# Kernel tuning notes

Measured on AMD Instinct MI355X. Metric: run time of the kernel, lower is better.

## Reference

```python
import jax, jax.numpy as jnp
import numpy as np

B, N, C = 8, 4096, 512
H = 8
OUT = 512
DH = C // H  # 64
LN_EPS = 1e-5
L2_EPS = 1e-12


def setup_inputs() -> dict:
    key = jax.random.key(0)
    ks = jax.random.split(key, 6)
    x = jax.random.normal(ks[0], (B, N, C), dtype=jnp.float32)
    ln_g = jnp.ones((C,), dtype=jnp.float32)
    ln_b = jnp.zeros((C,), dtype=jnp.float32)
    qkv_w = jax.random.normal(ks[1], (3 * C, C), dtype=jnp.float32) * 0.02  # torch Linear weight [out,in]
    temperature = jnp.ones((H, 1, 1), dtype=jnp.float32)
    proj_w = jax.random.normal(ks[2], (OUT, C), dtype=jnp.float32) * 0.02
    proj_b = jnp.zeros((OUT,), dtype=jnp.float32)
    return {"x": x, "ln_g": ln_g, "ln_b": ln_b, "qkv_w": qkv_w,
            "temperature": temperature, "proj_w": proj_w, "proj_b": proj_b}


def reference(x, ln_g, ln_b, qkv_w, temperature, proj_w, proj_b):
    # LayerNorm
    mu = jnp.mean(x, axis=-1, keepdims=True)
    var = jnp.mean(jnp.square(x - mu), axis=-1, keepdims=True)
    xn = (x - mu) * jax.lax.rsqrt(var + LN_EPS) * ln_g + ln_b
    # QKV projection (no bias)
    qkv = xn @ qkv_w.T  # [B,N,3C]
    qkv = qkv.reshape(B, N, 3, H, DH).transpose(2, 0, 3, 4, 1)  # [3,B,H,DH,N]
    q, k, v = qkv[0], qkv[1], qkv[2]  # each [B,H,DH,N] (already 'transposed' channel layout)
    # L2-normalize q,k along token dim (matches F.normalize eps behavior)
    q = q / jnp.clip(jnp.linalg.norm(q, axis=-1, keepdims=True), L2_EPS)
    k = k / jnp.clip(jnp.linalg.norm(k, axis=-1, keepdims=True), L2_EPS)
    # channel attention [B,H,DH,DH], scaled by per-head temperature
    attn = jnp.einsum('bhdn,bhen->bhde', q, k) * temperature[None]
    attn = jax.nn.softmax(attn, axis=-1)
    out = jnp.einsum('bhde,bhen->bhdn', attn, v)  # [B,H,DH,N]
    out = out.transpose(0, 3, 1, 2).reshape(B, N, H * DH)  # [B,N,C]
    out = jax.nn.gelu(out, approximate=False)
    out = out @ proj_w.T + proj_b
    return out
```

## Files before the change

### kernel.cpp

```cpp
#include <hip/hip_runtime.h>
#include <hip/hip_bf16.h>

typedef __hip_bfloat16 bf16;
typedef __bf16 bfrag __attribute__((ext_vector_type(8)));
typedef float f32x4 __attribute__((ext_vector_type(4)));

#define AS1 __attribute__((address_space(1)))
#define AS3 __attribute__((address_space(3)))

static constexpr int Bb = 8, Nn = 4096, Cc = 512, Hh = 8;
static constexpr int Mtok = Bb * Nn;
static constexpr int QKVC = 3 * Cc;
static constexpr size_t WS_NEED = 57147392;

__device__ __forceinline__ void gl_lds16(const void* g, void* l) {
  __builtin_amdgcn_global_load_lds((const AS1 void*)g, (AS3 void*)l, 16, 0, 0);
}
__device__ __forceinline__ float gelu_exact(float x) {
  return 0.5f * x * (1.0f + erff(x * 0.70710678118654752f));
}
__device__ __forceinline__ int g3(int x) { return ((x & 1) << 2) | (x >> 1); }

__global__ __launch_bounds__(256) void fill_f32(float* o, float val, int n) {
  int i = blockIdx.x * 256 + threadIdx.x;
  if (i < n) o[i] = val;
}

__global__ __launch_bounds__(256) void cvt_f32_bf16(const float* __restrict__ a,
                                                    bf16* __restrict__ o, int n) {
  int i = (blockIdx.x * 256 + threadIdx.x) * 8;
  if (i + 8 <= n) {
    float f[8];
    *(float4*)f       = *(const float4*)(a + i);
    *(float4*)(f + 4) = *(const float4*)(a + i + 4);
    bf16 v[8];
#pragma unroll
    for (int j = 0; j < 8; ++j) v[j] = __float2bfloat16(f[j]);
    *(uint4*)(o + i) = *(uint4*)v;
  }
}

__global__ __launch_bounds__(256) void cvt_mirror(const float* __restrict__ Gcov,
                                                  bf16* __restrict__ Gcvb) {
  int tile = blockIdx.x, b = blockIdx.y;
  int ti = tile >> 2, tj = tile & 3;
  int t = threadIdx.x;
  const float* gb = Gcov + (size_t)b * Cc * Cc;
  bf16* ob = Gcvb + (size_t)b * Cc * Cc;
  if (ti <= tj) {
#pragma unroll
    for (int r8 = 0; r8 < 8; ++r8) {
      int row = r8 * 16 + (t >> 4), col = (t & 15) * 8;
      const float* src = gb + (size_t)(ti * 128 + row) * Cc + tj * 128 + col;
      float f[8];
      *(float4*)f       = *(const float4*)src;
      *(float4*)(f + 4) = *(const float4*)(src + 4);
      bf16 v[8];
#pragma unroll
      for (int j = 0; j < 8; ++j) v[j] = __float2bfloat16(f[j]);
      *(uint4*)(ob + (size_t)(ti * 128 + row) * Cc + tj * 128 + col) = *(uint4*)v;
    }
  } else {
    __shared__ bf16 ls[128][136];
#pragma unroll
    for (int r8 = 0; r8 < 8; ++r8) {
      int srow = r8 * 16 + (t >> 4), scol = (t & 15) * 8;
      const float* src = gb + (size_t)(tj * 128 + srow) * Cc + ti * 128 + scol;
      float f[8];
      *(float4*)f       = *(const float4*)src;
      *(float4*)(f + 4) = *(const float4*)(src + 4);
      bf16 v[8];
#pragma unroll
      for (int j = 0; j < 8; ++j) v[j] = __float2bfloat16(f[j]);
      *(uint4*)&ls[srow][scol] = *(uint4*)v;
    }
    __syncthreads();
#pragma unroll
    for (int r8 = 0; r8 < 8; ++r8) {
      int orow = r8 * 16 + (t >> 4), ocol = (t & 15) * 8;
      bf16 v[8];
#pragma unroll
      for (int u = 0; u < 8; ++u) v[u] = ls[ocol + u][orow];
      *(uint4*)(ob + (size_t)(ti * 128 + orow) * Cc + tj * 128 + ocol) = *(uint4*)v;
    }
  }
}

__global__ __launch_bounds__(256) void ln_kernel(const float* __restrict__ x,
                                                 const float* __restrict__ gw,
                                                 const float* __restrict__ bw,
                                                 bf16* __restrict__ xn) {
  int tok  = blockIdx.x * 4 + (threadIdx.x >> 6);
  int lane = threadIdx.x & 63;
  const float* xr = x + (size_t)tok * Cc + lane * 8;
  float f[8];
  *(float4*)f       = *(const float4*)xr;
  *(float4*)(f + 4) = *(const float4*)(xr + 4);
  float s = 0.f;
#pragma unroll
  for (int j = 0; j < 8; ++j) s += f[j];
#pragma unroll
  for (int m = 32; m; m >>= 1) s += __shfl_xor(s, m);
  float mu = s * (1.0f / 512.0f);
  float q = 0.f;
#pragma unroll
  for (int j = 0; j < 8; ++j) { float d = f[j] - mu; q += d * d; }
#pragma unroll
  for (int m = 32; m; m >>= 1) q += __shfl_xor(q, m);
  float rstd = rsqrtf(q * (1.0f / 512.0f) + 1e-5f);
  bf16 o[8];
#pragma unroll
  for (int j = 0; j < 8; ++j)
    o[j] = __float2bfloat16((f[j] - mu) * rstd * gw[lane * 8 + j] + bw[lane * 8 + j]);
  *(uint4*)(xn + (size_t)tok * Cc + lane * 8) = *(uint4*)o;
}

template <typename TC, bool SWZ>
__global__ __launch_bounds__(256) void gemm_bt(const bf16* __restrict__ A,
                                               const bf16* __restrict__ B,
                                               TC* __restrict__ C,
                                               int M, int N, int K,
                                               const float* __restrict__ bias,
                                               long sA_z, long sB_z, long sC_z) {
  A += (size_t)blockIdx.z * sA_z;
  B += (size_t)blockIdx.z * sB_z;
  C += (size_t)blockIdx.z * sC_z;
  __shared__ __align__(16) bf16 smem[16384];
  bf16* sA = smem;
  bf16* sB = smem + 8192;
  int t = threadIdx.x, w = t >> 6, lane = t & 63, fr = lane & 15, quad = lane >> 4;
  int n0, m0;
  if constexpr (SWZ) {
    int flat = blockIdx.y * 4 + blockIdx.x;
    int idx  = (flat & 7) * 128 + (flat >> 3);
    n0 = (idx & 3) * 128;
    m0 = (idx >> 2) * 128;
  } else {
    n0 = blockIdx.x * 128;
    m0 = blockIdx.y * 128;
  }
  int wm = (w >> 1) * 64, wn = (w & 1) * 64;
  f32x4 acc[4][4] = {};

  for (int k0 = 0; k0 < K; k0 += 64) {
    __syncthreads();
#pragma unroll
    for (int c2 = 0; c2 < 4; ++c2) {
      int c = w * 4 + c2;
      int row = c * 8 + (lane >> 3);
      int ke  = ((lane & 7) ^ (lane >> 3)) * 8;
      gl_lds16(A + (size_t)(m0 + row) * K + k0 + ke, (char*)sA + c * 1024);
      gl_lds16(B + (size_t)(n0 + row) * K + k0 + ke, (char*)sB + c * 1024);
    }
    __syncthreads();
#pragma unroll
    for (int kk = 0; kk < 64; kk += 32) {
      bfrag af[4], bg[4];
#pragma unroll
      for (int i = 0; i < 4; ++i)
        af[i] = *(const bfrag*)(sA + (wm + i * 16 + fr) * 64 +
                                ((((kk >> 3) + quad) ^ (fr & 7)) * 8));
#pragma unroll
      for (int j = 0; j < 4; ++j)
        bg[j] = *(const bfrag*)(sB + (wn + j * 16 + fr) * 64 +
                                ((((kk >> 3) + quad) ^ (fr & 7)) * 8));
#pragma unroll
      for (int i = 0; i < 4; ++i)
#pragma unroll
        for (int j = 0; j < 4; ++j)
          acc[i][j] = __builtin_amdgcn_mfma_f32_16x16x32_bf16(af[i], bg[j], acc[i][j], 0, 0, 0);
    }
  }

  if constexpr (__is_same(TC, float)) {
#pragma unroll
    for (int j = 0; j < 4; ++j) {
      float bj = bias ? bias[n0 + wn + j * 16 + fr] : 0.0f;
#pragma unroll
      for (int i = 0; i < 4; ++i)
#pragma unroll
        for (int r = 0; r < 4; ++r)
          C[(size_t)(m0 + wm + i * 16 + quad * 4 + r) * N + n0 + wn + j * 16 + fr] =
              acc[i][j][r] + bj;
    }
  } else {
    __syncthreads();
    bf16* ct = smem;
#pragma unroll
    for (int j = 0; j < 4; ++j) {
      float bj = bias ? bias[n0 + wn + j * 16 + fr] : 0.0f;
#pragma unroll
      for (int i = 0; i < 4; ++i)
#pragma unroll
        for (int r = 0; r < 4; ++r)
          ct[(wm + i * 16 + quad * 4 + r) * 128 + wn + j * 16 + fr] =
              __float2bfloat16(acc[i][j][r] + bj);
    }
    __syncthreads();
#pragma unroll
    for (int r8 = 0; r8 < 8; ++r8) {
      int row = r8 * 16 + (t >> 4);
      int ce  = (t & 15) * 8;
      *(uint4*)(C + (size_t)(m0 + row) * N + n0 + ce) = *(const uint4*)(smem + row * 128 + ce);
    }
  }
}

__global__ __launch_bounds__(256) void xtx(const bf16* __restrict__ xn,
                                           float* __restrict__ Gcov) {
  int flat = blockIdx.x;
  int idx  = (flat & 7) * 80 + (flat >> 3);
  int tile = idx % 10;
  int sb   = idx / 10;
  int split = sb & 7, b = sb >> 3;
  int tm = tile < 4 ? 0 : tile < 7 ? 1 : tile < 9 ? 2 : 3;
  int tn = tile < 4 ? tile : tile < 7 ? tile - 3 : tile < 9 ? tile - 5 : 3;
  int m0 = tm * 128, n0 = tn * 128;
  bool diag = (m0 == n0);
  int t = threadIdx.x, w = t >> 6, lane = t & 63, fr = lane & 15, quad = lane >> 4;
  int wm = (w >> 1) * 64, wn = (w & 1) * 64;
  __shared__ __align__(16) bf16 sA[8192], sB[8192];
  const bf16* sBp = diag ? sA : sB;
  f32x4 acc[4][4] = {};
  const bf16* xb = xn + ((size_t)b * Nn + split * 512) * Cc;
  int ch0 = (t & 15) * 8;
  int tg  = t >> 4;
  int swz = g3(t & 7);
  unsigned wpos = (((unsigned)((tg >> 1) ^ swz)) * 16u) + (unsigned)(tg & 1) * 8u;
  uint4 va[4], vb[4];
#pragma unroll
  for (int j = 0; j < 4; ++j) {
    int tk = tg * 4 + j;
    va[j] = *(const uint4*)(xb + (size_t)tk * Cc + m0 + ch0);
    if (!diag) vb[j] = *(const uint4*)(xb + (size_t)tk * Cc + n0 + ch0);
  }
  for (int kc = 0; kc < 8; ++kc) {
    __syncthreads();
#pragma unroll
    for (int k = 0; k < 4; ++k) {
      unsigned a0 = ((const unsigned*)&va[0])[k], a1 = ((const unsigned*)&va[1])[k];
      unsigned a2 = ((const unsigned*)&va[2])[k], a3 = ((const unsigned*)&va[3])[k];
      uint2 lo = { (a0 & 0xffffu) | (a1 << 16), (a2 & 0xffffu) | (a3 << 16) };
      uint2 hi = { (a0 >> 16) | (a1 & 0xffff0000u), (a2 >> 16) | (a3 & 0xffff0000u) };
      *(uint2*)((char*)sA + (unsigned)(ch0 + 2 * k) * 128 + wpos) = lo;
      *(uint2*)((char*)sA + (unsigned)(ch0 + 2 * k + 1) * 128 + wpos) = hi;
      if (!diag) {
        unsigned b0 = ((const unsigned*)&vb[0])[k], b1 = ((const unsigned*)&vb[1])[k];
        unsigned b2 = ((const unsigned*)&vb[2])[k], b3 = ((const unsigned*)&vb[3])[k];
        uint2 lo2 = { (b0 & 0xffffu) | (b1 << 16), (b2 & 0xffffu) | (b3 << 16) };
        uint2 hi2 = { (b0 >> 16) | (b1 & 0xffff0000u), (b2 >> 16) | (b3 & 0xffff0000u) };
        *(uint2*)((char*)sB + (unsigned)(ch0 + 2 * k) * 128 + wpos) = lo2;
        *(uint2*)((char*)sB + (unsigned)(ch0 + 2 * k + 1) * 128 + wpos) = hi2;
      }
    }
    __syncthreads();
    if (kc < 7) {
      const bf16* xb2 = xb + (size_t)(kc + 1) * 64 * Cc;
#pragma unroll
      for (int j = 0; j < 4; ++j) {
        int tk = tg * 4 + j;
        va[j] = *(const uint4*)(xb2 + (size_t)tk * Cc + m0 + ch0);
        if (!diag) vb[j] = *(const uint4*)(xb2 + (size_t)tk * Cc + n0 + ch0);
      }
    }
#pragma unroll
    for (int s = 0; s < 2; ++s) {
      bfrag af[4], bg[4];
#pragma unroll
      for (int i = 0; i < 4; ++i) {
        int ch = wm + i * 16 + fr;
        int blk = (s * 4 + quad) ^ g3((ch >> 3) & 7);
        af[i] = *(const bfrag*)(sA + ch * 64 + blk * 8);
      }
#pragma unroll
      for (int j = 0; j < 4; ++j) {
        int ch = wn + j * 16 + fr;
        int blk = (s * 4 + quad) ^ g3((ch >> 3) & 7);
        bg[j] = *(const bfrag*)(sBp + ch * 64 + blk * 8);
      }
#pragma unroll
      for (int i = 0; i < 4; ++i)
#pragma unroll
        for (int j = 0; j < 4; ++j)
          acc[i][j] = __builtin_amdgcn_mfma_f32_16x16x32_bf16(af[i], bg[j], acc[i][j], 0, 0, 0);
    }
  }
  float* gb = Gcov + (size_t)b * Cc * Cc;
#pragma unroll
  for (int i = 0; i < 4; ++i)
#pragma unroll
    for (int j = 0; j < 4; ++j)
#pragma unroll
      for (int r = 0; r < 4; ++r)
        atomicAdd(&gb[(size_t)(m0 + wm + i * 16 + quad * 4 + r) * Cc + n0 + wn + j * 16 + fr],
                  acc[i][j][r]);
}

__global__ __launch_bounds__(256) void gram_softmax(const bf16* __restrict__ T,
                                                    const bf16* __restrict__ wq,
                                                    const float* __restrict__ temp,
                                                    bf16* __restrict__ P) {
  int h = blockIdx.x, b = blockIdx.y;
  int t = threadIdx.x, w = t >> 6, lane = t & 63, fr = lane & 15, quad = lane >> 4;
  const bf16* Tq = T + (size_t)b * 1024 * 512 + (size_t)(h * 64) * 512;
  const bf16* Tk = T + (size_t)b * 1024 * 512 + (size_t)(512 + h * 64) * 512;
  const bf16* Wqh = wq + (size_t)(h * 64) * 512;
  const bf16* Wkh = wq + (size_t)(512 + h * 64) * 512;
  f32x4 acc[4][4] = {};
#pragma unroll
  for (int s = 0; s < 4; ++s) {
    int kb = w * 128 + s * 32 + quad * 8;
    bfrag af[4], bg[4];
#pragma unroll
    for (int i = 0; i < 4; ++i) af[i] = *(const bfrag*)(Tq + (size_t)(i * 16 + fr) * 512 + kb);
#pragma unroll
    for (int j = 0; j < 4; ++j) bg[j] = *(const bfrag*)(Wkh + (size_t)(j * 16 + fr) * 512 + kb);
#pragma unroll
    for (int i = 0; i < 4; ++i)
#pragma unroll
      for (int j = 0; j < 4; ++j)
        acc[i][j] = __builtin_amdgcn_mfma_f32_16x16x32_bf16(af[i], bg[j], acc[i][j], 0, 0, 0);
  }
  __shared__ float parts[4 * 4096];
  __shared__ float nrm[2][4][64];
  __shared__ float nqk[2][64];
#pragma unroll
  for (int i = 0; i < 4; ++i)
#pragma unroll
    for (int j = 0; j < 4; ++j)
#pragma unroll
      for (int r = 0; r < 4; ++r)
        parts[w * 4096 + (i * 16 + quad * 4 + r) * 64 + j * 16 + fr] = acc[i][j][r];
  {
    int d = t & 63, qtr = t >> 6, c0 = qtr * 128;
    float pq = 0.f, pk = 0.f;
#pragma unroll 4
    for (int cc = 0; cc < 16; ++cc) {
      bf16 a[8], ww[8];
      *(uint4*)a  = *(const uint4*)(Tq + (size_t)d * 512 + c0 + cc * 8);
      *(uint4*)ww = *(const uint4*)(Wqh + (size_t)d * 512 + c0 + cc * 8);
#pragma unroll
      for (int j = 0; j < 8; ++j) pq += __bfloat162float(a[j]) * __bfloat162float(ww[j]);
      *(uint4*)a  = *(const uint4*)(Tk + (size_t)d * 512 + c0 + cc * 8);
      *(uint4*)ww = *(const uint4*)(Wkh + (size_t)d * 512 + c0 + cc * 8);
#pragma unroll
      for (int j = 0; j < 8; ++j) pk += __bfloat162float(a[j]) * __bfloat162float(ww[j]);
    }
    nrm[0][qtr][d] = pq;
    nrm[1][qtr][d] = pk;
  }
  __syncthreads();
  if (t < 64) {
    nqk[0][t] = fmaxf(sqrtf(nrm[0][0][t] + nrm[0][1][t] + nrm[0][2][t] + nrm[0][3][t]), 1e-12f);
    nqk[1][t] = fmaxf(sqrtf(nrm[1][0][t] + nrm[1][1][t] + nrm[1][2][t] + nrm[1][3][t]), 1e-12f);
  }
  __syncthreads();
  if (t < 64) {
    int d = t;
    float sc = temp[h] / nqk[0][d];
    float l[64]; float mx = -1e30f;
#pragma unroll
    for (int e = 0; e < 64; ++e) {
      float vsum = parts[d * 64 + e] + parts[4096 + d * 64 + e] +
                   parts[8192 + d * 64 + e] + parts[12288 + d * 64 + e];
      l[e] = vsum * sc / nqk[1][e];
      mx = fmaxf(mx, l[e]);
    }
    float sum = 0.f;
#pragma unroll
    for (int e = 0; e < 64; ++e) { l[e] = expf(l[e] - mx); sum += l[e]; }
    float inv = 1.0f / sum;
    bf16* pr = P + ((size_t)(b * 8 + h) * 64 + d) * 64;
#pragma unroll
    for (int e = 0; e < 64; ++e) pr[e] = __float2bfloat16(l[e] * inv);
  }
}

__global__ __launch_bounds__(256) void pv_gelu(const bf16* __restrict__ P,
                                               const bf16* __restrict__ v,
                                               bf16* __restrict__ g) {
  int chunk = blockIdx.x, h = blockIdx.y, b = blockIdx.z;
  int t = threadIdx.x, w = t >> 6, lane = t & 63, fr = lane & 15, quad = lane >> 4;
  const bf16* pb = P + (size_t)(b * 8 + h) * 4096;
  bfrag pf[4][2];
#pragma unroll
  for (int i = 0; i < 4; ++i)
#pragma unroll
    for (int c = 0; c < 2; ++c)
      pf[i][c] = *(const bfrag*)(pb + (i * 16 + fr) * 64 + c * 32 + quad * 8);
#pragma unroll 2
  for (int nt = 0; nt < 8; ++nt) {
    int ntok = chunk * 512 + w * 128 + nt * 16 + fr;
    const bf16* vrow = v + (size_t)(b * Nn + ntok) * Cc + h * 64 + quad * 8;
    bfrag bv0 = *(const bfrag*)(vrow);
    bfrag bv1 = *(const bfrag*)(vrow + 32);
    f32x4 acc[4] = {};
#pragma unroll
    for (int i = 0; i < 4; ++i) {
      acc[i] = __builtin_amdgcn_mfma_f32_16x16x32_bf16(pf[i][0], bv0, acc[i], 0, 0, 0);
      acc[i] = __builtin_amdgcn_mfma_f32_16x16x32_bf16(pf[i][1], bv1, acc[i], 0, 0, 0);
    }
    bf16* grow = g + (size_t)(b * Nn + ntok) * Cc + h * 64;
#pragma unroll
    for (int i = 0; i < 4; ++i) {
      bf16 o[4];
#pragma unroll
      for (int r = 0; r < 4; ++r) o[r] = __float2bfloat16(gelu_exact(acc[i][r]));
      *(uint2*)(grow + i * 16 + quad * 4) = *(uint2*)o;
    }
  }
}

extern "C" void kernel_launch(void* const* d_in, const int* in_sizes, int n_in,
                              void* d_out, int out_size, void* d_ws, size_t ws_size,
                              hipStream_t stream) {
  const float* x      = (const float*)d_in[0];
  const float* ln_g   = (const float*)d_in[1];
  const float* ln_b   = (const float*)d_in[2];
  const float* qkv_w  = (const float*)d_in[3];
  const float* temp   = (const float*)d_in[4];
  const float* proj_w = (const float*)d_in[5];
  const float* proj_b = (const float*)d_in[6];
  float* out = (float*)d_out;
  char*  ws  = (char*)d_ws;

  const int exp_sizes[7] = {16777216, 512, 512, 786432, 8, 262144, 512};
  bool sizes_ok = (n_in == 7) && (out_size == 16777216);
  if (sizes_ok) for (int i = 0; i < 7; ++i) sizes_ok = sizes_ok && (in_sizes[i] == exp_sizes[i]);
  if (!sizes_ok) {
    fill_f32<<<(16777216 + 255) / 256, 256, 0, stream>>>(out, 500.0f, out_size);
    return;
  }
  if (ws_size < WS_NEED) {
    fill_f32<<<(16777216 + 255) / 256, 256, 0, stream>>>(out, (float)(ws_size >> 20), out_size);
    return;
  }

  bf16*  xn   = (bf16*)ws;
  bf16*  g    = (bf16*)ws;
  float* Gcov = (float*)(ws + 33554432);
  bf16*  Gcvb = (bf16*)(ws + 41943040);
  bf16*  T    = (bf16*)(ws + 46137344);
  bf16*  P    = (bf16*)(ws + 54525952);
  bf16*  wq   = (bf16*)(ws + 55050240);
  bf16*  wp   = (bf16*)(ws + 56623104);
  bf16*  v    = (bf16*)d_out;

  cvt_f32_bf16<<<384, 256, 0, stream>>>(qkv_w, wq, QKVC * Cc);
  cvt_f32_bf16<<<128, 256, 0, stream>>>(proj_w, wp, Cc * Cc);
  hipMemsetAsync(Gcov, 0, (size_t)Bb * Cc * Cc * sizeof(float), stream);
  ln_kernel<<<Mtok / 4, 256, 0, stream>>>(x, ln_g, ln_b, xn);
  gemm_bt<bf16, true><<<dim3(4, 256, 1), 256, 0, stream>>>(xn, wq + 1024 * 512, v, Mtok, Cc, Cc,
                                                           nullptr, 0, 0, 0);
  xtx<<<640, 256, 0, stream>>>(xn, Gcov);
  cvt_mirror<<<dim3(16, 8), 256, 0, stream>>>(Gcov, Gcvb);
  gemm_bt<bf16, false><<<dim3(4, 8, 8), 256, 0, stream>>>(wq, Gcvb, T, 1024, Cc, Cc,
                                                          nullptr, 0, (long)Cc * Cc, (long)1024 * Cc);
  gram_softmax<<<dim3(Hh, Bb), 256, 0, stream>>>(T, wq, temp, P);
  pv_gelu<<<dim3(8, Hh, Bb), 256, 0, stream>>>(P, v, g);
  gemm_bt<float, true><<<dim3(4, 256, 1), 256, 0, stream>>>(g, wp, out, Mtok, Cc, Cc,
                                                            proj_b, 0, 0, 0);
}
```

Measured before the change: 276.0 us.

## Retile xtx covariance kernel to 64x128 lower-triangular tiles with fewer token splits

```diff
diff --git a/kernel.cpp b/kernel.cpp
--- a/kernel.cpp
+++ b/kernel.cpp
@@ -210,78 +210,86 @@
                                            float* __restrict__ Gcov) {
   int flat = blockIdx.x;
   int idx  = (flat & 7) * 80 + (flat >> 3);
-  int tile = idx % 10;
-  int sb   = idx / 10;
-  int split = sb & 7, b = sb >> 3;
-  int tm = tile < 4 ? 0 : tile < 7 ? 1 : tile < 9 ? 2 : 3;
-  int tn = tile < 4 ? tile : tile < 7 ? tile - 3 : tile < 9 ? tile - 5 : 3;
-  int m0 = tm * 128, n0 = tn * 128;
-  bool diag = (m0 == n0);
+  int tile = idx % 20;
+  int sb   = idx / 20;
+  int split = sb & 3, b = sb >> 2;
+  int nt = tile < 2 ? 0 : tile < 6 ? 1 : tile < 12 ? 2 : 3;
+  int mt = tile - (nt == 0 ? 0 : nt == 1 ? 2 : nt == 2 ? 6 : 12);
+  int m0 = mt * 64, n0 = nt * 128;
+  bool alias = ((mt >> 1) == nt);
   int t = threadIdx.x, w = t >> 6, lane = t & 63, fr = lane & 15, quad = lane >> 4;
-  int wm = (w >> 1) * 64, wn = (w & 1) * 64;
-  __shared__ __align__(16) bf16 sA[8192], sB[8192];
-  const bf16* sBp = diag ? sA : sB;
-  f32x4 acc[4][4] = {};
-  const bf16* xb = xn + ((size_t)b * Nn + split * 512) * Cc;
-  int ch0 = (t & 15) * 8;
-  int tg  = t >> 4;
-  int swz = g3(t & 7);
-  unsigned wpos = (((unsigned)((tg >> 1) ^ swz)) * 16u) + (unsigned)(tg & 1) * 8u;
+  int wn = w * 32;
+  __shared__ __align__(16) bf16 sB[8192];
+  __shared__ __align__(16) bf16 sAb[4096];
+  bf16* sA = alias ? (sB + (mt & 1) * 4096) : sAb;
+  f32x4 acc[4][2] = {};
+  const bf16* xb = xn + ((size_t)b * Nn + split * 1024) * Cc;
+  int ch0b = (t & 15) * 8, tgb = t >> 4;
+  int ch0a = (t & 7) * 8,  tga = t >> 3;
+  bool doA = (!alias) && (t < 128);
+  unsigned swz = (unsigned)g3(t & 7);
+  unsigned wposb = (((unsigned)(tgb >> 1) ^ swz) * 16u) + (unsigned)(tgb & 1) * 8u;
+  unsigned wposa = (((unsigned)(tga >> 1) ^ swz) * 16u) + (unsigned)(tga & 1) * 8u;
   uint4 va[4], vb[4];
 #pragma unroll
-  for (int j = 0; j < 4; ++j) {
-    int tk = tg * 4 + j;
-    va[j] = *(const uint4*)(xb + (size_t)tk * Cc + m0 + ch0);
-    if (!diag) vb[j] = *(const uint4*)(xb + (size_t)tk * Cc + n0 + ch0);
-  }
-  for (int kc = 0; kc < 8; ++kc) {
+  for (int j = 0; j < 4; ++j)
+    vb[j] = *(const uint4*)(xb + (size_t)(tgb * 4 + j) * Cc + n0 + ch0b);
+  if (doA)
+#pragma unroll
+    for (int j = 0; j < 4; ++j)
+      va[j] = *(const uint4*)(xb + (size_t)(tga * 4 + j) * Cc + m0 + ch0a);
+  for (int kc = 0; kc < 16; ++kc) {
     __syncthreads();
 #pragma unroll
     for (int k = 0; k < 4; ++k) {
-      unsigned a0 = ((const unsigned*)&va[0])[k], a1 = ((const unsigned*)&va[1])[k];
-      unsigned a2 = ((const unsigned*)&va[2])[k], a3 = ((const unsigned*)&va[3])[k];
-      uint2 lo = { (a0 & 0xffffu) | (a1 << 16), (a2 & 0xffffu) | (a3 << 16) };
-      uint2 hi = { (a0 >> 16) | (a1 & 0xffff0000u), (a2 >> 16) | (a3 & 0xffff0000u) };
-      *(uint2*)((char*)sA + (unsigned)(ch0 + 2 * k) * 128 + wpos) = lo;
-      *(uint2*)((char*)sA + (unsigned)(ch0 + 2 * k + 1) * 128 + wpos) = hi;
-      if (!diag) {
-        unsigned b0 = ((const unsigned*)&vb[0])[k], b1 = ((const unsigned*)&vb[1])[k];
-        unsigned b2 = ((const unsigned*)&vb[2])[k], b3 = ((const unsigned*)&vb[3])[k];
-        uint2 lo2 = { (b0 & 0xffffu) | (b1 << 16), (b2 & 0xffffu) | (b3 << 16) };
-        uint2 hi2 = { (b0 >> 16) | (b1 & 0xffff0000u), (b2 >> 16) | (b3 & 0xffff0000u) };
-        *(uint2*)((char*)sB + (unsigned)(ch0 + 2 * k) * 128 + wpos) = lo2;
-        *(uint2*)((char*)sB + (unsigned)(ch0 + 2 * k + 1) * 128 + wpos) = hi2;
+      unsigned b0 = ((const unsigned*)&vb[0])[k], b1 = ((const unsigned*)&vb[1])[k];
+      unsigned b2 = ((const unsigned*)&vb[2])[k], b3 = ((const unsigned*)&vb[3])[k];
+      uint2 lo = { (b0 & 0xffffu) | (b1 << 16), (b2 & 0xffffu) | (b3 << 16) };
+      uint2 hi = { (b0 >> 16) | (b1 & 0xffff0000u), (b2 >> 16) | (b3 & 0xffff0000u) };
+      *(uint2*)((char*)sB + (unsigned)(ch0b + 2 * k) * 128 + wposb) = lo;
+      *(uint2*)((char*)sB + (unsigned)(ch0b + 2 * k + 1) * 128 + wposb) = hi;
+    }
+    if (doA) {
+#pragma unroll
+      for (int k = 0; k < 4; ++k) {
+        unsigned a0 = ((const unsigned*)&va[0])[k], a1 = ((const unsigned*)&va[1])[k];
+        unsigned a2 = ((const unsigned*)&va[2])[k], a3 = ((const unsigned*)&va[3])[k];
+        uint2 lo = { (a0 & 0xffffu) | (a1 << 16), (a2 & 0xffffu) | (a3 << 16) };
+        uint2 hi = { (a0 >> 16) | (a1 & 0xffff0000u), (a2 >> 16) | (a3 & 0xffff0000u) };
+        *(uint2*)((char*)sAb + (unsigned)(ch0a + 2 * k) * 128 + wposa) = lo;
+        *(uint2*)((char*)sAb + (unsigned)(ch0a + 2 * k + 1) * 128 + wposa) = hi;
       }
     }
     __syncthreads();
-    if (kc < 7) {
+    if (kc < 15) {
       const bf16* xb2 = xb + (size_t)(kc + 1) * 64 * Cc;
 #pragma unroll
-      for (int j = 0; j < 4; ++j) {
-        int tk = tg * 4 + j;
-        va[j] = *(const uint4*)(xb2 + (size_t)tk * Cc + m0 + ch0);
-        if (!diag) vb[j] = *(const uint4*)(xb2 + (size_t)tk * Cc + n0 + ch0);
+      for (int j = 0; j < 4; ++j)
+        vb[j] = *(const uint4*)(xb2 + (size_t)(tgb * 4 + j) * Cc + n0 + ch0b);
+      if (doA)
+#pragma unroll
+        for (int j = 0; j < 4; ++j)
+          va[j] = *(const uint4*)(xb2 + (size_t)(tga * 4 + j) * Cc + m0 + ch0a);
+    }
+#pragma unroll
+    for (int kk = 0; kk < 2; ++kk) {
+      bfrag af[4], bg[2];
+#pragma unroll
+      for (int i = 0; i < 4; ++i) {
+        int ch = i * 16 + fr;
+        int slot = (kk * 4 + quad) ^ g3((ch >> 3) & 7);
+        af[i] = *(const bfrag*)(sA + ch * 64 + slot * 8);
       }
-    }
-#pragma unroll
-    for (int s = 0; s < 2; ++s) {
-      bfrag af[4], bg[4];
-#pragma unroll
-      for (int i = 0; i < 4; ++i) {
-        int ch = wm + i * 16 + fr;
-        int blk = (s * 4 + quad) ^ g3((ch >> 3) & 7);
-        af[i] = *(const bfrag*)(sA + ch * 64 + blk * 8);
+#pragma unroll
+      for (int j = 0; j < 2; ++j) {
+        int ch = wn + j * 16 + fr;
+        int slot = (kk * 4 + quad) ^ g3((ch >> 3) & 7);
+        bg[j] = *(const bfrag*)(sB + ch * 64 + slot * 8);
       }
 #pragma unroll
-      for (int j = 0; j < 4; ++j) {
-        int ch = wn + j * 16 + fr;
-        int blk = (s * 4 + quad) ^ g3((ch >> 3) & 7);
-        bg[j] = *(const bfrag*)(sBp + ch * 64 + blk * 8);
-      }
-#pragma unroll
       for (int i = 0; i < 4; ++i)
 #pragma unroll
-        for (int j = 0; j < 4; ++j)
+        for (int j = 0; j < 2; ++j)
           acc[i][j] = __builtin_amdgcn_mfma_f32_16x16x32_bf16(af[i], bg[j], acc[i][j], 0, 0, 0);
     }
   }
@@ -289,10 +297,10 @@
 #pragma unroll
   for (int i = 0; i < 4; ++i)
 #pragma unroll
-    for (int j = 0; j < 4; ++j)
+    for (int j = 0; j < 2; ++j)
 #pragma unroll
       for (int r = 0; r < 4; ++r)
-        atomicAdd(&gb[(size_t)(m0 + wm + i * 16 + quad * 4 + r) * Cc + n0 + wn + j * 16 + fr],
+        atomicAdd(&gb[(size_t)(m0 + i * 16 + quad * 4 + r) * Cc + n0 + wn + j * 16 + fr],
                   acc[i][j][r]);
 }
 
```

After: 265.3 us. -3.9%, faster.
